# Kernel optimization log

Measured on AMD Instinct MI355X. Metric: run time of the kernel, lower is better.

Reference implementation:

```python
import math
import jax, jax.numpy as jnp
import numpy as np


def setup_inputs() -> dict:
    key = jax.random.key(0)
    ks = jax.random.split(key, 8)
    N, Lv, M, Lt = 4096, 16, 4096, 77
    Din, D, R = 512, 768, 4  # fc in-dim, model dim, bottleneck ratio
    Dh = D // R
    s = lambda k, shape, fan_in: jax.random.normal(k, shape, jnp.float32) * (1.0 / math.sqrt(fan_in))
    return {
        "vision_prompt": jax.random.normal(ks[0], (N, Lv, D), jnp.float32),
        "text_prompt": jax.random.normal(ks[1], (M, Lt, Din), jnp.float32),
        "fc_w": s(ks[2], (D, Din), Din),        # torch Linear layout [out, in]
        "fc_b": jnp.zeros((D,), jnp.float32),
        "ln_g": jnp.ones((D,), jnp.float32),
        "ln_b": jnp.zeros((D,), jnp.float32),
        "mlp_w1": s(ks[3], (Dh, D), D),
        "mlp_b1": jnp.zeros((Dh,), jnp.float32),
        "mlp_w2": s(ks[4], (D, Dh), Dh),
        "mlp_b2": jnp.zeros((D,), jnp.float32),
    }


def _layernorm(x, g, b, eps=1e-5):
    mu = jnp.mean(x, axis=-1, keepdims=True)
    var = jnp.var(x, axis=-1, keepdims=True)
    return (x - mu) * jax.lax.rsqrt(var + eps) * g + b


def reference(vision_prompt, text_prompt, fc_w, fc_b, ln_g, ln_b,
              mlp_w1, mlp_b1, mlp_w2, mlp_b2):
    N, Lv, D = vision_prompt.shape
    mean_v = jnp.mean(vision_prompt, axis=1)                    # [N, D]
    mean_t = jnp.mean(text_prompt, axis=1)                      # [M, Din]
    t = mean_t @ fc_w.T + fc_b                                  # [M, D]
    scores = jnp.einsum('nc,mc->nm', mean_v, t) / math.sqrt(D)  # [N, M]
    aff = jax.nn.softmax(scores, axis=-1)
    agg = jnp.einsum('nm,mc->nc', aff, t)                       # [N, D]
    h = _layernorm(agg, ln_g, ln_b)
    h = jax.nn.relu(h @ mlp_w1.T + mlp_b1)
    h = h @ mlp_w2.T + mlp_b2                                   # [N, D]
    return jnp.broadcast_to(h[:, None, :], (N, Lv, D))
```

## Files before the change

kernel.cpp:

```cpp
#include <hip/hip_runtime.h>
#include <math.h>

typedef unsigned short u16;
typedef __attribute__((ext_vector_type(4))) float f32x4;
typedef __attribute__((ext_vector_type(8))) short bf16x8;

#define GLOBAL_AS __attribute__((address_space(1)))
#define LDS_AS __attribute__((address_space(3)))

__device__ __forceinline__ u16 f2bf(float f) {
  unsigned u = __builtin_bit_cast(unsigned, f);
  unsigned lsb = (u >> 16) & 1u;
  u += 0x7fffu + lsb;
  return (u16)(u >> 16);
}

__device__ __forceinline__ float bf2f(u16 b) {
  return __builtin_bit_cast(float, ((unsigned)b) << 16);
}

__device__ __forceinline__ void gload16(const void* g, void* l) {
  __builtin_amdgcn_global_load_lds((const GLOBAL_AS void*)g, (LDS_AS void*)l, 16, 0, 0);
}

__global__ __launch_bounds__(256) void prologue_kernel(
    const float* __restrict__ vision, const float* __restrict__ text,
    const float* __restrict__ fc_w, const float* __restrict__ w1,
    const float* __restrict__ w2, const float* __restrict__ b1,
    u16* __restrict__ mean_v, u16* __restrict__ mean_t,
    u16* __restrict__ fcw_bf, u16* __restrict__ w1p, u16* __restrict__ w2p,
    float* __restrict__ b1p)
{
  const int n_mv = 4096 * 192;
  const int n_mt = 4096 * 128;
  const int n_fcw = 768 * 512;
  const int n_w1 = 256 * 768;
  const int n_w2 = 768 * 256;
  int id = blockIdx.x * 256 + threadIdx.x;

  if (id < n_mv) {
    int n = id / 192, c = id % 192;
    const f32x4* x = (const f32x4*)vision + (size_t)n * 16 * 192 + c;
    f32x4 s = {0.f, 0.f, 0.f, 0.f};
#pragma unroll
    for (int l = 0; l < 16; ++l) s += x[(size_t)l * 192];
    s *= (1.f / 16.f);
    ushort4 o; o.x = f2bf(s.x); o.y = f2bf(s.y); o.z = f2bf(s.z); o.w = f2bf(s.w);
    ((ushort4*)mean_v)[id] = o;
    return;
  }
  id -= n_mv;
  if (id < n_mt) {
    int n = id / 128, c = id % 128;
    const f32x4* x = (const f32x4*)text + (size_t)n * 77 * 128 + c;
    f32x4 s = {0.f, 0.f, 0.f, 0.f};
    for (int l = 0; l < 77; ++l) s += x[(size_t)l * 128];
    s *= (1.f / 77.f);
    ushort4 o; o.x = f2bf(s.x); o.y = f2bf(s.y); o.z = f2bf(s.z); o.w = f2bf(s.w);
    ((ushort4*)mean_t)[id] = o;
    return;
  }
  id -= n_mt;
  if (id < n_fcw) { fcw_bf[id] = f2bf(fc_w[id]); return; }
  id -= n_fcw;
  if (id < n_w1) {
    int r = id / 768;
    w1p[id] = (r < 192) ? f2bf(w1[id]) : (u16)0;
    return;
  }
  id -= n_w1;
  if (id < n_w2) {
    int r = id / 256, c = id % 256;
    w2p[id] = (c < 192) ? f2bf(w2[(size_t)r * 192 + c]) : (u16)0;
    return;
  }
  id -= n_w2;
  if (id < 256) b1p[id] = (id < 192) ? b1[id] : 0.f;
}

__global__ __launch_bounds__(512, 2) void gemm256_exp_bf16(
    const u16* __restrict__ A, const u16* __restrict__ B, float alpha,
    u16* __restrict__ C, float* __restrict__ dsum, int N, int K, int lda, int ldb)
{
  __shared__ u16 lA[3][256 * 32];
  __shared__ u16 lB[3][256 * 32];
  const int tid = threadIdx.x;
  const int w = tid >> 6, lane = tid & 63;
  const int brow = blockIdx.y * 256, bcol = blockIdx.x * 256;
  const int wr = w >> 2, wc = w & 3;

  f32x4 acc[8][4];
#pragma unroll
  for (int i = 0; i < 8; ++i)
#pragma unroll
    for (int j = 0; j < 4; ++j) acc[i][j] = (f32x4){0.f, 0.f, 0.f, 0.f};

  const int srow = lane >> 2;
  const int scol = (lane & 3) * 8;
  const size_t ga0 = (size_t)(brow + (w * 2 + 0) * 16 + srow) * lda + scol;
  const size_t ga1 = (size_t)(brow + (w * 2 + 1) * 16 + srow) * lda + scol;
  const size_t gb0 = (size_t)(bcol + (w * 2 + 0) * 16 + srow) * ldb + scol;
  const size_t gb1 = (size_t)(bcol + (w * 2 + 1) * 16 + srow) * ldb + scol;

  const int fr = lane & 15, fk = (lane >> 4) * 8;
  const int NT = K >> 5;

  auto stage = [&](int ti, int b) {
    const int k0 = ti << 5;
    char* la = (char*)&lA[b][0] + w * 2048;
    char* lb = (char*)&lB[b][0] + w * 2048;
    gload16(A + ga0 + k0, la);
    gload16(A + ga1 + k0, la + 1024);
    gload16(B + gb0 + k0, lb);
    gload16(B + gb1 + k0, lb + 1024);
  };

  stage(0, 0);
  stage(1, 1);

  int bR = 0;
  for (int it = 0; it < NT; ++it) {
    if (it + 1 < NT) { asm volatile("s_waitcnt vmcnt(4)" ::: "memory"); }
    else             { asm volatile("s_waitcnt vmcnt(0)" ::: "memory"); }
    __builtin_amdgcn_s_barrier();
    asm volatile("" ::: "memory");

    int bW = bR + 2; if (bW >= 3) bW -= 3;
    if (it + 2 < NT) stage(it + 2, bW);

    const u16* la = lA[bR];
    const u16* lb = lB[bR];
    bf16x8 av[8], bv[4];
#pragma unroll
    for (int mi = 0; mi < 8; ++mi)
      av[mi] = *(const bf16x8*)&la[(wr * 128 + mi * 16 + fr) * 32 + fk];
#pragma unroll
    for (int ni = 0; ni < 4; ++ni)
      bv[ni] = *(const bf16x8*)&lb[(wc * 64 + ni * 16 + fr) * 32 + fk];

    __builtin_amdgcn_s_setprio(1);
#pragma unroll
    for (int mi = 0; mi < 8; ++mi)
#pragma unroll
      for (int ni = 0; ni < 4; ++ni)
        acc[mi][ni] = __builtin_amdgcn_mfma_f32_16x16x32_bf16(av[mi], bv[ni], acc[mi][ni], 0, 0, 0);
    __builtin_amdgcn_s_setprio(0);

    bR = (bR + 1 == 3) ? 0 : bR + 1;
  }

  const int fq = lane >> 4;
  float rsum[8][4];
#pragma unroll
  for (int mi = 0; mi < 8; ++mi)
#pragma unroll
    for (int r = 0; r < 4; ++r) rsum[mi][r] = 0.f;

#pragma unroll
  for (int mi = 0; mi < 8; ++mi) {
#pragma unroll
    for (int ni = 0; ni < 4; ++ni) {
      int col = bcol + wc * 64 + ni * 16 + fr;
#pragma unroll
      for (int r = 0; r < 4; ++r) {
        int row = brow + wr * 128 + mi * 16 + fq * 4 + r;
        float v = __expf(acc[mi][ni][r] * alpha);
        C[(size_t)row * N + col] = f2bf(v);
        rsum[mi][r] += v;
      }
    }
  }
#pragma unroll
  for (int mi = 0; mi < 8; ++mi)
#pragma unroll
    for (int r = 0; r < 4; ++r) {
      float s = rsum[mi][r];
      s += __shfl_xor(s, 1); s += __shfl_xor(s, 2);
      s += __shfl_xor(s, 4); s += __shfl_xor(s, 8);
      rsum[mi][r] = s;
    }
  __syncthreads();
  float* wsum = (float*)&lA[0][0];
  if (fr == 0) {
#pragma unroll
    for (int mi = 0; mi < 8; ++mi)
#pragma unroll
      for (int r = 0; r < 4; ++r)
        wsum[wc * 256 + wr * 128 + mi * 16 + fq * 4 + r] = rsum[mi][r];
  }
  __syncthreads();
  if (tid < 256) {
    float s = wsum[tid] + wsum[256 + tid] + wsum[512 + tid] + wsum[768 + tid];
    dsum[(size_t)(brow + tid) * 16 + blockIdx.x] = s;
  }
}

template<bool RELU, bool BF16OUT, bool TRANST, bool BCAST16>
__global__ __launch_bounds__(256) void gemm_nt(
    const u16* __restrict__ A, const u16* __restrict__ B,
    const float* __restrict__ bias, float alpha,
    float* __restrict__ Cf, u16* __restrict__ Cb,
    u16* __restrict__ Ct, int ldt,
    int M, int N, int K, int lda, int ldb,
    int kofs, long long cofs)
{
  __shared__ char lds[49152];
  const int t = threadIdx.x;
  const int w = t >> 6, lane = t & 63;
  const int brow = blockIdx.y * 128, bcol = blockIdx.x * 128;
  const int wr = w >> 1, wc = w & 1;
  const int kz = blockIdx.z;

  A += (size_t)kz * kofs;
  B += (size_t)kz * kofs;
  Cf += kz * cofs;

  f32x4 acc[4][4];
#pragma unroll
  for (int i = 0; i < 4; ++i)
#pragma unroll
    for (int j = 0; j < 4; ++j) acc[i][j] = (f32x4){0.f, 0.f, 0.f, 0.f};

  const int srow = t >> 2;
  const int scol = (t & 3) * 8;
  const size_t aoff0 = (size_t)(brow + srow) * lda + scol;
  const size_t boff0 = (size_t)(bcol + srow) * ldb + scol;
  const size_t aoff1 = aoff0 + (size_t)64 * lda;
  const size_t boff1 = boff0 + (size_t)64 * ldb;

  const int fr = lane & 15, fk = (lane >> 4) * 8;
  const int NT = K >> 5;

  auto stage = [&](int ti, int b) {
    const int k0 = ti << 5;
    char* la = lds + b * 16384 + w * 1024;
    char* lb = lds + b * 16384 + 8192 + w * 1024;
    gload16(A + aoff0 + k0, la);
    gload16(A + aoff1 + k0, la + 4096);
    gload16(B + boff0 + k0, lb);
    gload16(B + boff1 + k0, lb + 4096);
  };

  stage(0, 0);
  stage(1, 1);

  int bR = 0;
  for (int it = 0; it < NT; ++it) {
    if (it + 1 < NT) { asm volatile("s_waitcnt vmcnt(4)" ::: "memory"); }
    else             { asm volatile("s_waitcnt vmcnt(0)" ::: "memory"); }
    __builtin_amdgcn_s_barrier();
    asm volatile("" ::: "memory");

    int bW = bR + 2; if (bW >= 3) bW -= 3;
    if (it + 2 < NT) stage(it + 2, bW);

    const u16* la = (const u16*)(lds + bR * 16384);
    const u16* lb = (const u16*)(lds + bR * 16384 + 8192);
    bf16x8 av[4], bv[4];
#pragma unroll
    for (int mi = 0; mi < 4; ++mi)
      av[mi] = *(const bf16x8*)&la[(wr * 64 + mi * 16 + fr) * 32 + fk];
#pragma unroll
    for (int ni = 0; ni < 4; ++ni)
      bv[ni] = *(const bf16x8*)&lb[(wc * 64 + ni * 16 + fr) * 32 + fk];

    __builtin_amdgcn_s_setprio(1);
#pragma unroll
    for (int mi = 0; mi < 4; ++mi)
#pragma unroll
      for (int ni = 0; ni < 4; ++ni)
        acc[mi][ni] = __builtin_amdgcn_mfma_f32_16x16x32_bf16(av[mi], bv[ni], acc[mi][ni], 0, 0, 0);
    __builtin_amdgcn_s_setprio(0);

    bR = (bR + 1 == 3) ? 0 : bR + 1;
  }

  const int fq = lane >> 4;
  u16* tileT = (u16*)lds;
  if (TRANST) __syncthreads();

#pragma unroll
  for (int mi = 0; mi < 4; ++mi) {
#pragma unroll
    for (int ni = 0; ni < 4; ++ni) {
      int cl = wc * 64 + ni * 16 + fr;
      int col = bcol + cl;
      float bb = bias ? bias[col] : 0.f;
#pragma unroll
      for (int r = 0; r < 4; ++r) {
        int rl = wr * 64 + mi * 16 + fq * 4 + r;
        int row = brow + rl;
        float v = acc[mi][ni][r] * alpha + bb;
        if (RELU) v = fmaxf(v, 0.f);
        if (BF16OUT) {
          u16 bf = f2bf(v);
          Cb[(size_t)row * N + col] = bf;
          if (TRANST) tileT[cl * 130 + rl] = bf;
        } else if (BCAST16) {
          size_t b0 = ((size_t)row * 16) * (size_t)N + col;
#pragma unroll
          for (int l = 0; l < 16; ++l) Cf[b0 + (size_t)l * N] = v;
        } else {
          Cf[(size_t)row * N + col] = v;
        }
      }
    }
  }

  if (TRANST) {
    __syncthreads();
    int c2 = t >> 1, off = (t & 1) * 64;
    size_t base = (size_t)(bcol + c2) * ldt + brow + off;
#pragma unroll
    for (int j = 0; j < 8; ++j)
      *(bf16x8*)&Ct[base + j * 8] = *(const bf16x8*)&tileT[c2 * 130 + off + j * 8];
  }
}

__global__ __launch_bounds__(256) void ln4_kernel(
    const float* __restrict__ X, long long ps, const float* __restrict__ dsum,
    const float* __restrict__ g, const float* __restrict__ b,
    u16* __restrict__ Y)
{
  __shared__ float red[4];
  int row = blockIdx.x, t = threadIdx.x;
  const float* x = X + (size_t)row * 768;
  float s16 = 0.f;
#pragma unroll
  for (int j = 0; j < 16; ++j) s16 += dsum[(size_t)row * 16 + j];
  float inv_d = 1.f / s16;

  float v0 = (x[t]       + x[ps + t]       + x[2 * ps + t]       + x[3 * ps + t]) * inv_d;
  float v1 = (x[t + 256] + x[ps + t + 256] + x[2 * ps + t + 256] + x[3 * ps + t + 256]) * inv_d;
  float v2 = (x[t + 512] + x[ps + t + 512] + x[2 * ps + t + 512] + x[3 * ps + t + 512]) * inv_d;

  float s = v0 + v1 + v2;
#pragma unroll
  for (int off = 32; off > 0; off >>= 1) s += __shfl_xor(s, off);
  if ((t & 63) == 0) red[t >> 6] = s;
  __syncthreads();
  float mu = (red[0] + red[1] + red[2] + red[3]) * (1.f / 768.f);
  __syncthreads();

  float d0 = v0 - mu, d1 = v1 - mu, d2 = v2 - mu;
  float q = d0 * d0 + d1 * d1 + d2 * d2;
#pragma unroll
  for (int off = 32; off > 0; off >>= 1) q += __shfl_xor(q, off);
  if ((t & 63) == 0) red[t >> 6] = q;
  __syncthreads();
  float var = (red[0] + red[1] + red[2] + red[3]) * (1.f / 768.f);
  float inv = rsqrtf(var + 1e-5f);

  u16* y = Y + (size_t)row * 768;
  y[t]       = f2bf(d0 * inv * g[t]       + b[t]);
  y[t + 256] = f2bf(d1 * inv * g[t + 256] + b[t + 256]);
  y[t + 512] = f2bf(d2 * inv * g[t + 512] + b[t + 512]);
}

extern "C" void kernel_launch(void* const* d_in, const int* in_sizes, int n_in,
                              void* d_out, int out_size, void* d_ws, size_t ws_size,
                              hipStream_t stream)
{
  const float* vision = (const float*)d_in[0];
  const float* text   = (const float*)d_in[1];
  const float* fc_w   = (const float*)d_in[2];
  const float* fc_b   = (const float*)d_in[3];
  const float* ln_g   = (const float*)d_in[4];
  const float* ln_b   = (const float*)d_in[5];
  const float* w1     = (const float*)d_in[6];
  const float* b1     = (const float*)d_in[7];
  const float* w2     = (const float*)d_in[8];
  const float* b2     = (const float*)d_in[9];
  float* out = (float*)d_out;

  const int N = 4096, M = 4096, Din = 512, D = 768, Dhp = 256;

  char* p = (char*)d_ws;
  auto alloc = [&](size_t bytes) { char* r = p; p += (bytes + 255) & ~(size_t)255; return r; };
  u16*   mean_v = (u16*)alloc((size_t)N * D * 2);
  u16*   mean_t = (u16*)alloc((size_t)M * Din * 2);
  u16*   fcw_bf = (u16*)alloc((size_t)D * Din * 2);
  u16*   w1p    = (u16*)alloc((size_t)Dhp * D * 2);
  u16*   w2p    = (u16*)alloc((size_t)D * Dhp * 2);
  float* b1p    = (float*)alloc((size_t)Dhp * 4);
  float* dsum   = (float*)alloc((size_t)N * 16 * 4);
  u16*   t_bf   = (u16*)alloc((size_t)M * D * 2);
  u16*   tT_bf  = (u16*)alloc((size_t)D * M * 2);
  u16*   aff    = (u16*)alloc((size_t)N * M * 2);
  u16*   ln_o   = (u16*)alloc((size_t)N * D * 2);
  u16*   h1     = (u16*)alloc((size_t)N * Dhp * 2);
  float* aggp   = (float*)alloc((size_t)4 * N * D * 4);

  {
    int total = 4096 * 192 + 4096 * 128 + 768 * 512 + 256 * 768 + 768 * 256 + 256;
    prologue_kernel<<<(total + 255) / 256, 256, 0, stream>>>(
        vision, text, fc_w, w1, w2, b1, mean_v, mean_t, fcw_bf, w1p, w2p, b1p);
  }

  gemm_nt<false, true, true, false><<<dim3(D / 128, M / 128), 256, 0, stream>>>(
      mean_t, fcw_bf, fc_b, 1.f, nullptr, t_bf, tT_bf, M, M, D, Din, Din, Din, 0, 0);

  gemm256_exp_bf16<<<dim3(M / 256, N / 256), 512, 0, stream>>>(
      mean_v, t_bf, 1.f / sqrtf(768.f), aff, dsum, M, D, D, D);

  gemm_nt<false, false, false, false><<<dim3(D / 128, N / 128, 4), 256, 0, stream>>>(
      aff, tT_bf, nullptr, 1.f, aggp, nullptr, nullptr, 0, N, D, M / 4, M, M,
      M / 4, (long long)N * D);

  ln4_kernel<<<N, 256, 0, stream>>>(aggp, (long long)N * D, dsum, ln_g, ln_b, ln_o);

  gemm_nt<true, true, false, false><<<dim3(Dhp / 128, N / 128), 256, 0, stream>>>(
      ln_o, w1p, b1p, 1.f, nullptr, h1, nullptr, 0, N, Dhp, D, D, D, 0, 0);

  gemm_nt<false, false, false, true><<<dim3(D / 128, N / 128), 256, 0, stream>>>(
      h1, w2p, b2, 1.f, out, nullptr, nullptr, 0, N, D, Dhp, Dhp, Dhp, 0, 0);
}
```

Measured before the change: 385.3 us.

## Stage exp-GEMM output through LDS, swizzle block order, vectorize small loads

The exp/score GEMM epilogue now writes bf16 results into an LDS tile and stores them as coalesced 16-byte rows, replacing scattered 2-byte global stores. Both GEMM kernels remap block indices with an interleaving swizzle, aiming for better L2 reuse across concurrently running blocks. The text-mean loop is unrolled, and the layernorm kernel reads its partial denominators with vector loads. The LDS round-trip in the epilogue adds extra barriers, and the swizzle assumes the block count divides evenly by 8.

```diff
diff --git a/kernel.cpp b/kernel.cpp
--- a/kernel.cpp
+++ b/kernel.cpp
@@ -54,6 +54,7 @@
     int n = id / 128, c = id % 128;
     const f32x4* x = (const f32x4*)text + (size_t)n * 77 * 128 + c;
     f32x4 s = {0.f, 0.f, 0.f, 0.f};
+#pragma unroll 7
     for (int l = 0; l < 77; ++l) s += x[(size_t)l * 128];
     s *= (1.f / 77.f);
     ushort4 o; o.x = f2bf(s.x); o.y = f2bf(s.y); o.z = f2bf(s.z); o.w = f2bf(s.w);
@@ -82,11 +83,16 @@
     const u16* __restrict__ A, const u16* __restrict__ B, float alpha,
     u16* __restrict__ C, float* __restrict__ dsum, int N, int K, int lda, int ldb)
 {
-  __shared__ u16 lA[3][256 * 32];
-  __shared__ u16 lB[3][256 * 32];
+  __shared__ char lds[98304];
   const int tid = threadIdx.x;
   const int w = tid >> 6, lane = tid & 63;
-  const int brow = blockIdx.y * 256, bcol = blockIdx.x * 256;
+
+  const int gx = gridDim.x;
+  const int nb = gx * gridDim.y;
+  int b0 = blockIdx.y * gx + blockIdx.x;
+  int swz = (b0 & 7) * (nb >> 3) + (b0 >> 3);
+  const int bx = swz % gx, by = swz / gx;
+  const int brow = by * 256, bcol = bx * 256;
   const int wr = w >> 2, wc = w & 3;
 
   f32x4 acc[8][4];
@@ -107,8 +113,8 @@
 
   auto stage = [&](int ti, int b) {
     const int k0 = ti << 5;
-    char* la = (char*)&lA[b][0] + w * 2048;
-    char* lb = (char*)&lB[b][0] + w * 2048;
+    char* la = lds + b * 16384 + w * 2048;
+    char* lb = lds + 49152 + b * 16384 + w * 2048;
     gload16(A + ga0 + k0, la);
     gload16(A + ga1 + k0, la + 1024);
     gload16(B + gb0 + k0, lb);
@@ -128,8 +134,8 @@
     int bW = bR + 2; if (bW >= 3) bW -= 3;
     if (it + 2 < NT) stage(it + 2, bW);
 
-    const u16* la = lA[bR];
-    const u16* lb = lB[bR];
+    const u16* la = (const u16*)(lds + bR * 16384);
+    const u16* lb = (const u16*)(lds + 49152 + bR * 16384);
     bf16x8 av[8], bv[4];
 #pragma unroll
     for (int mi = 0; mi < 8; ++mi)
@@ -150,25 +156,21 @@
   }
 
   const int fq = lane >> 4;
+  __syncthreads();
+
   float rsum[8][4];
 #pragma unroll
-  for (int mi = 0; mi < 8; ++mi)
+  for (int mi = 0; mi < 8; ++mi) {
 #pragma unroll
     for (int r = 0; r < 4; ++r) rsum[mi][r] = 0.f;
-
-#pragma unroll
-  for (int mi = 0; mi < 8; ++mi) {
-#pragma unroll
-    for (int ni = 0; ni < 4; ++ni) {
-      int col = bcol + wc * 64 + ni * 16 + fr;
+#pragma unroll
+    for (int ni = 0; ni < 4; ++ni)
 #pragma unroll
       for (int r = 0; r < 4; ++r) {
-        int row = brow + wr * 128 + mi * 16 + fq * 4 + r;
         float v = __expf(acc[mi][ni][r] * alpha);
-        C[(size_t)row * N + col] = f2bf(v);
+        acc[mi][ni][r] = v;
         rsum[mi][r] += v;
       }
-    }
   }
 #pragma unroll
   for (int mi = 0; mi < 8; ++mi)
@@ -179,8 +181,7 @@
       s += __shfl_xor(s, 4); s += __shfl_xor(s, 8);
       rsum[mi][r] = s;
     }
-  __syncthreads();
-  float* wsum = (float*)&lA[0][0];
+  float* wsum = (float*)(lds + 73728);
   if (fr == 0) {
 #pragma unroll
     for (int mi = 0; mi < 8; ++mi)
@@ -188,10 +189,38 @@
       for (int r = 0; r < 4; ++r)
         wsum[wc * 256 + wr * 128 + mi * 16 + fq * 4 + r] = rsum[mi][r];
   }
-  __syncthreads();
+
+  u16* tile = (u16*)lds;
+#pragma unroll
+  for (int s = 0; s < 2; ++s) {
+    if ((wc >> 1) == s) {
+#pragma unroll
+      for (int mi = 0; mi < 8; ++mi)
+#pragma unroll
+        for (int ni = 0; ni < 4; ++ni) {
+          int cc = (wc & 1) * 64 + ni * 16 + fr;
+#pragma unroll
+          for (int r = 0; r < 4; ++r) {
+            int rr = wr * 128 + mi * 16 + fq * 4 + r;
+            tile[rr * 136 + cc] = f2bf(acc[mi][ni][r]);
+          }
+        }
+    }
+    __syncthreads();
+    {
+      int row = tid >> 1, part = tid & 1;
+      size_t base = (size_t)(brow + row) * N + bcol + s * 128 + part * 64;
+      const u16* tr = &tile[row * 136 + part * 64];
+#pragma unroll
+      for (int j = 0; j < 8; ++j)
+        *(bf16x8*)&C[base + j * 8] = *(const bf16x8*)&tr[j * 8];
+    }
+    __syncthreads();
+  }
+
   if (tid < 256) {
     float s = wsum[tid] + wsum[256 + tid] + wsum[512 + tid] + wsum[768 + tid];
-    dsum[(size_t)(brow + tid) * 16 + blockIdx.x] = s;
+    dsum[(size_t)(brow + tid) * 16 + bx] = s;
   }
 }
 
@@ -207,9 +236,17 @@
   __shared__ char lds[49152];
   const int t = threadIdx.x;
   const int w = t >> 6, lane = t & 63;
-  const int brow = blockIdx.y * 128, bcol = blockIdx.x * 128;
+
+  const int gx = gridDim.x, gy = gridDim.y;
+  const int nb = gx * gy * gridDim.z;
+  int b0 = (blockIdx.z * gy + blockIdx.y) * gx + blockIdx.x;
+  int swz = (b0 & 7) * (nb >> 3) + (b0 >> 3);
+  const int bx = swz % gx;
+  int tmp = swz / gx;
+  const int by = tmp % gy, kz = tmp / gy;
+
+  const int brow = by * 128, bcol = bx * 128;
   const int wr = w >> 1, wc = w & 1;
-  const int kz = blockIdx.z;
 
   A += (size_t)kz * kofs;
   B += (size_t)kz * kofs;
@@ -297,9 +334,9 @@
           Cb[(size_t)row * N + col] = bf;
           if (TRANST) tileT[cl * 130 + rl] = bf;
         } else if (BCAST16) {
-          size_t b0 = ((size_t)row * 16) * (size_t)N + col;
-#pragma unroll
-          for (int l = 0; l < 16; ++l) Cf[b0 + (size_t)l * N] = v;
+          size_t b0o = ((size_t)row * 16) * (size_t)N + col;
+#pragma unroll
+          for (int l = 0; l < 16; ++l) Cf[b0o + (size_t)l * N] = v;
         } else {
           Cf[(size_t)row * N + col] = v;
         }
@@ -325,10 +362,9 @@
   __shared__ float red[4];
   int row = blockIdx.x, t = threadIdx.x;
   const float* x = X + (size_t)row * 768;
-  float s16 = 0.f;
-#pragma unroll
-  for (int j = 0; j < 16; ++j) s16 += dsum[(size_t)row * 16 + j];
-  float inv_d = 1.f / s16;
+  const f32x4* dv = (const f32x4*)(dsum + (size_t)row * 16);
+  f32x4 d4 = dv[0] + dv[1] + dv[2] + dv[3];
+  float inv_d = 1.f / (d4.x + d4.y + d4.z + d4.w);
 
   float v0 = (x[t]       + x[ps + t]       + x[2 * ps + t]       + x[3 * ps + t]) * inv_d;
   float v1 = (x[t + 256] + x[ps + t + 256] + x[2 * ps + t + 256] + x[3 * ps + t + 256]) * inv_d;
```

Result: no change. 379.1 us (-1.6%).
